# Performance work log

Measured on AMD Instinct MI355X. Metric: run time of the kernel, lower is better.

Reference implementation:

```python
import jax, jax.numpy as jnp
import numpy as np

T, B, C, H, W = 128, 16, 4, 84, 84
NUM_ACTIONS, FEAT, HID = 18, 512, 256


def _conv(x, w, b, stride):
    # x: (N,C,H,W), w: (O,I,kh,kw)
    y = jax.lax.conv_general_dilated(
        x, w, window_strides=(stride, stride), padding='VALID',
        dimension_numbers=('NCHW', 'OIHW', 'NCHW'))
    return y + b[None, :, None, None]


def setup_inputs() -> dict:
    key = jax.random.key(0)
    ks = jax.random.split(key, 24)
    s = 0.05
    inp = {
        'obs_seq': jax.random.uniform(ks[0], (T, B, C, H, W), jnp.float32) * 255.0,
        'actions_seq': jax.random.randint(ks[1], (T, B), 0, NUM_ACTIONS),
        'episode_starts_seq': jax.random.randint(ks[2], (T, B), 0, 2).astype(jnp.float32),
        'h0': jnp.zeros((1, B, HID), jnp.float32),
        'c0': jnp.zeros((1, B, HID), jnp.float32),
        # NatureCNN params
        'conv1_w': jax.random.normal(ks[3], (32, C, 8, 8)) * s,
        'conv1_b': jnp.zeros((32,)),
        'conv2_w': jax.random.normal(ks[4], (64, 32, 4, 4)) * s,
        'conv2_b': jnp.zeros((64,)),
        'conv3_w': jax.random.normal(ks[5], (64, 64, 3, 3)) * s,
        'conv3_b': jnp.zeros((64,)),
        'fc_w': jax.random.normal(ks[6], (FEAT, 64 * 7 * 7)) * s,
        'fc_b': jnp.zeros((FEAT,)),
        # LSTM params (torch gate order i,f,g,o)
        'w_ih': jax.random.normal(ks[7], (4 * HID, FEAT)) * s,
        'w_hh': jax.random.normal(ks[8], (4 * HID, HID)) * s,
        'b_ih': jnp.zeros((4 * HID,)),
        'b_hh': jnp.zeros((4 * HID,)),
        # heads
        'actor_w': jax.random.normal(ks[9], (NUM_ACTIONS, HID)) * 0.01,
        'actor_b': jnp.zeros((NUM_ACTIONS,)),
        'critic_w': jax.random.normal(ks[10], (1, HID)) * s,
        'critic_b': jnp.zeros((1,)),
        'aux_w': jax.random.normal(ks[11], (1, FEAT)) * s,
        'aux_b': jnp.zeros((1,)),
    }
    return inp


def reference(obs_seq, actions_seq, episode_starts_seq, h0, c0,
              conv1_w, conv1_b, conv2_w, conv2_b, conv3_w, conv3_b,
              fc_w, fc_b, w_ih, w_hh, b_ih, b_hh,
              actor_w, actor_b, critic_w, critic_b, aux_w, aux_b):
    t, b = actions_seq.shape
    x = obs_seq.reshape(t * b, *obs_seq.shape[2:]) / 255.0
    x = jax.nn.relu(_conv(x, conv1_w, conv1_b, 4))   # (TB,32,20,20)
    x = jax.nn.relu(_conv(x, conv2_w, conv2_b, 2))   # (TB,64,9,9)
    x = jax.nn.relu(_conv(x, conv3_w, conv3_b, 1))   # (TB,64,7,7)
    feat = jax.nn.relu(x.reshape(t * b, -1) @ fc_w.T + fc_b)  # (TB,FEAT)

    aux_logits = (feat @ aux_w.T + aux_b).squeeze(-1).reshape(t, b)
    feat_seq = feat.reshape(t, b, -1)

    def step(carry, inp):
        h, c = carry
        x_t, s_t = inp
        keep = (1.0 - s_t)[:, None]
        h = h * keep
        c = c * keep
        gates = x_t @ w_ih.T + b_ih + h @ w_hh.T + b_hh  # (B,4H)
        i, f, g, o = jnp.split(gates, 4, axis=-1)
        c = jax.nn.sigmoid(f) * c + jax.nn.sigmoid(i) * jnp.tanh(g)
        h = jax.nn.sigmoid(o) * jnp.tanh(c)
        return (h, c), h

    _, out = jax.lax.scan(step, (h0[0], c0[0]), (feat_seq, episode_starts_seq))  # (T,B,HID)

    logits = out @ actor_w.T + actor_b
    logp = jax.nn.log_softmax(logits, axis=-1)
    log_probs = jnp.take_along_axis(logp, actions_seq[..., None], axis=-1).squeeze(-1)
    entropy = -jnp.sum(jnp.exp(logp) * logp, axis=-1)
    values = (out @ critic_w.T + critic_b).squeeze(-1)
    return log_probs, entropy, values, aux_logits
```

## Files before the change

### kernel.cpp

```cpp
#include <hip/hip_runtime.h>
#include <hip/hip_bf16.h>
#include <cstddef>

typedef __attribute__((ext_vector_type(8))) short bf16x8;
typedef __attribute__((ext_vector_type(4))) float f32x4;

static constexpr size_t OFF_X1B   = 0;
static constexpr size_t OFF_X2B   = 52428800;
static constexpr size_t OFF_X3B   = 73662464;
static constexpr size_t OFF_FEATB = 86507520;
static constexpr size_t OFF_W2B   = 88604672;
static constexpr size_t OFF_W3B   = 88670208;
static constexpr size_t OFF_FCWB  = 88743936;
static constexpr size_t OFF_WIHB  = 91955200;
static constexpr size_t OFF_FEAT  = 93003776;
static constexpr size_t OFF_GX    = 97198080;
static constexpr size_t OFF_HSEQ  = 105586688;
static constexpr size_t OFF_W1B   = 108732416;
static constexpr size_t OFF_WHHB  = 108748800;
static constexpr size_t OFF_ORDB  = 109273088;
static constexpr size_t OFF_ORDT0 = 109281280;
static constexpr size_t OFF_ORDLEN= 109289472;
static constexpr size_t OFF_NSEG  = 109297664;

__device__ __forceinline__ float sigmoidf_(float x) {
  return 1.0f / (1.0f + __expf(-x));
}
__device__ __forceinline__ float tanhf_(float x) {
  return 1.0f - 2.0f / (__expf(2.0f * x) + 1.0f);
}

__global__ __launch_bounds__(256) void prep_kernel(
    const float* __restrict__ c1w, const float* __restrict__ c2w,
    const float* __restrict__ c3w, const float* __restrict__ fcw,
    const float* __restrict__ wih, const float* __restrict__ whh,
    __hip_bfloat16* __restrict__ w1b,
    __hip_bfloat16* __restrict__ w2b, __hip_bfloat16* __restrict__ w3b,
    __hip_bfloat16* __restrict__ fcwb, __hip_bfloat16* __restrict__ wihb,
    __hip_bfloat16* __restrict__ whhb) {
  int i = blockIdx.x * 256 + threadIdx.x;
  if (i < 32768) {
    int o = i >> 9, k = i & 511;
    int pos = k >> 5, ci = k & 31;
    int ky = pos >> 2, kx = pos & 3;
    w2b[i] = __float2bfloat16(c2w[o * 512 + ci * 16 + ky * 4 + kx]);
  } else if (i < 69632) {
    int j = i - 32768;
    int o = j / 576, k = j - o * 576;
    int pos = k >> 6, ci = k & 63;
    int ky = pos / 3, kx = pos - ky * 3;
    w3b[j] = __float2bfloat16(c3w[o * 576 + ci * 9 + ky * 3 + kx]);
  } else if (i < 1675264) {
    int j = i - 69632;
    int o = j / 3136, k = j - o * 3136;
    int sp = k >> 6, ci = k & 63;
    fcwb[j] = __float2bfloat16(fcw[o * 3136 + ci * 49 + sp]);
  } else if (i < 2199552) {
    int j = i - 1675264;
    wihb[j] = __float2bfloat16(wih[j]);
  } else if (i < 2461696) {
    int j = i - 2199552;
    whhb[j] = __float2bfloat16(whh[j]);
  } else if (i < 2469888) {
    int j = i - 2461696;
    int oc = j >> 8, k = j & 255;
    int ky = k >> 5, rem = k & 31;
    int ci = rem >> 3, kx = rem & 7;
    w1b[j] = __float2bfloat16(c1w[oc * 256 + ci * 64 + ky * 8 + kx] * (1.0f / 255.0f));
  }
}

__global__ __launch_bounds__(256) void plan_kernel(
    const float* __restrict__ starts, int* __restrict__ ord_b,
    int* __restrict__ ord_t0, int* __restrict__ ord_len,
    int* __restrict__ nseg_out) {
  __shared__ int s_t0[2048];
  __shared__ int s_len[2048];
  __shared__ int cnt[16];
  __shared__ int hist[132];
  __shared__ int off[132];
  const int tid = threadIdx.x;
  if (tid < 16) {
    int b = tid, c = 0;
    for (int t = 0; t < 128; ++t) {
      float s = starts[t * 16 + b];
      if (t == 0 || s != 0.0f) {
        if (c > 0) s_len[b * 128 + c - 1] = t - s_t0[b * 128 + c - 1];
        s_t0[b * 128 + c] = t;
        ++c;
      }
    }
    s_len[b * 128 + c - 1] = 128 - s_t0[b * 128 + c - 1];
    cnt[b] = c;
  }
  if (tid < 132) hist[tid] = 0;
  __syncthreads();
  for (int idx = tid; idx < 2048; idx += 256) {
    int b = idx >> 7, i = idx & 127;
    if (i < cnt[b]) atomicAdd(&hist[s_len[idx]], 1);
  }
  __syncthreads();
  if (tid == 0) {
    int running = 0;
    for (int L = 128; L >= 1; --L) { off[L] = running; running += hist[L]; }
    *nseg_out = running;
  }
  __syncthreads();
  for (int idx = tid; idx < 2048; idx += 256) {
    int b = idx >> 7, i = idx & 127;
    if (i < cnt[b]) {
      int len = s_len[idx];
      int pos = atomicAdd(&off[len], 1);
      ord_b[pos] = b;
      ord_t0[pos] = s_t0[idx];
      ord_len[pos] = len;
    }
  }
}

__global__ __launch_bounds__(256) void conv1_mfma(
    const float* __restrict__ obs, const __hip_bfloat16* __restrict__ w1b,
    const float* __restrict__ b1, __hip_bfloat16* __restrict__ x1b) {
  constexpr int LDK = 40;
  __shared__ __align__(16) __hip_bfloat16 As[128 * LDK];
  __shared__ __align__(16) __hip_bfloat16 Ws[32 * LDK];
  const int tid = threadIdx.x;
  const int m0 = blockIdx.x * 128;
  const int l = tid & 63;
  const int wv = tid >> 6;
  const int lane16 = l & 15;
  const int quad = l >> 4;
  const int m_base = wv * 32;

  f32x4 acc[2][2] = {};

  const float* arow[2];
  int arw[2], acp[2];
#pragma unroll
  for (int c = 0; c < 2; ++c) {
    const int id = tid + c * 256;
    const int row = id >> 2, cpos = id & 3;
    arw[c] = row; acp[c] = cpos;
    const int m = m0 + row;
    const int n = m / 400, sp = m - n * 400;
    const int oy = sp / 20, ox = sp - oy * 20;
    arow[c] = obs + (size_t)n * 28224 + cpos * 7056 + (oy * 4) * 84 + ox * 4;
  }
  const int wrow = tid >> 2, wcp = tid & 3;
  const __hip_bfloat16* wsrc = w1b + wrow * 256 + wcp * 8;

  for (int s = 0; s < 8; ++s) {
    float4 p[2], q[2];
#pragma unroll
    for (int c = 0; c < 2; ++c) {
      const float* r = arow[c] + s * 84;
      p[c] = *(const float4*)r;
      q[c] = *(const float4*)(r + 4);
    }
    uint4 wval;
    if (tid < 128) wval = *(const uint4*)(wsrc + s * 32);
    __syncthreads();
#pragma unroll
    for (int c = 0; c < 2; ++c) {
      __hip_bfloat16* d = &As[arw[c] * LDK + acp[c] * 8];
      d[0] = __float2bfloat16(p[c].x); d[1] = __float2bfloat16(p[c].y);
      d[2] = __float2bfloat16(p[c].z); d[3] = __float2bfloat16(p[c].w);
      d[4] = __float2bfloat16(q[c].x); d[5] = __float2bfloat16(q[c].y);
      d[6] = __float2bfloat16(q[c].z); d[7] = __float2bfloat16(q[c].w);
    }
    if (tid < 128) *(uint4*)&Ws[wrow * LDK + wcp * 8] = wval;
    __syncthreads();
    const bf16x8 a0 = *(const bf16x8*)&As[(m_base + lane16) * LDK + quad * 8];
    const bf16x8 a1 = *(const bf16x8*)&As[(m_base + 16 + lane16) * LDK + quad * 8];
#pragma unroll
    for (int nf = 0; nf < 2; ++nf) {
      const bf16x8 b = *(const bf16x8*)&Ws[(nf * 16 + lane16) * LDK + quad * 8];
      acc[0][nf] = __builtin_amdgcn_mfma_f32_16x16x32_bf16(a0, b, acc[0][nf], 0, 0, 0);
      acc[1][nf] = __builtin_amdgcn_mfma_f32_16x16x32_bf16(a1, b, acc[1][nf], 0, 0, 0);
    }
  }
#pragma unroll
  for (int nf = 0; nf < 2; ++nf) {
    const int col = nf * 16 + lane16;
    const float bb = b1[col];
#pragma unroll
    for (int mf = 0; mf < 2; ++mf) {
#pragma unroll
      for (int r = 0; r < 4; ++r) {
        const int row = m0 + m_base + mf * 16 + quad * 4 + r;
        const float v = fmaxf(acc[mf][nf][r] + bb, 0.f);
        x1b[(size_t)row * 32 + col] = __float2bfloat16(v);
      }
    }
  }
}

template<int BM, int MODE>
__global__ __launch_bounds__(256) void gemm_mfma(
    const __hip_bfloat16* __restrict__ Abase,
    const __hip_bfloat16* __restrict__ Wb,
    const float* __restrict__ bias1, const float* __restrict__ bias2,
    float* __restrict__ Cf, __hip_bfloat16* __restrict__ Cb,
    const int M, const int N, const int K, const int relu) {
  constexpr int LDK = 40;
  __shared__ __align__(16) __hip_bfloat16 As[BM * LDK];
  __shared__ __align__(16) __hip_bfloat16 Ws[64 * LDK];
  const int tid = threadIdx.x;
  const int m0 = blockIdx.y * BM;
  const int n0 = blockIdx.x * 64;
  const int l = tid & 63;
  const int wv = tid >> 6;
  const int lane16 = l & 15;
  const int quad = l >> 4;
  constexpr int NF = (BM == 128) ? 4 : 2;
  const int m_base = (BM == 128) ? wv * 32 : (wv & 1) * 32;
  const int n_base = (BM == 128) ? 0 : (wv >> 1) * 32;
  constexpr int NCA = (BM == 128) ? 2 : 1;

  f32x4 acc[2][NF] = {};

  const __hip_bfloat16* arow[NCA];
  int acp[NCA];
#pragma unroll
  for (int c = 0; c < NCA; ++c) {
    const int id = tid + c * 256;
    const int row = id >> 2, cpos = id & 3;
    const int m = m0 + row;
    acp[c] = cpos;
    if (MODE == 0) {
      arow[c] = Abase + (size_t)m * K + cpos * 8;
    } else if (MODE == 1) {
      const int n = m / 81, sp = m - n * 81;
      const int oy = sp / 9, ox = sp - oy * 9;
      arow[c] = Abase + ((n * 20 + oy * 2) * 20 + ox * 2) * 32 + cpos * 8;
    } else {
      const int n = m / 49, sp = m - n * 49;
      const int oy = sp / 7, ox = sp - oy * 7;
      arow[c] = Abase + ((n * 9 + oy) * 9 + ox) * 64 + cpos * 8;
    }
  }
  const int wrow = tid >> 2, wcp = tid & 3;
  const __hip_bfloat16* wsrc = Wb + (size_t)(n0 + wrow) * K + wcp * 8;

  const int ksteps = K >> 5;
  for (int s = 0; s < ksteps; ++s) {
    uint4 av[NCA];
#pragma unroll
    for (int c = 0; c < NCA; ++c) {
      const __hip_bfloat16* p;
      if (MODE == 0) {
        p = arow[c] + s * 32;
      } else if (MODE == 1) {
        p = arow[c] + ((s >> 2) * 20 + (s & 3)) * 32;
      } else {
        const int pos = s >> 1;
        const int ky = pos / 3, kx = pos - ky * 3;
        p = arow[c] + (ky * 9 + kx) * 64 + (s & 1) * 32;
      }
      av[c] = *(const uint4*)p;
    }
    const uint4 wval = *(const uint4*)(wsrc + s * 32);
    __syncthreads();
#pragma unroll
    for (int c = 0; c < NCA; ++c) {
      const int row = (tid + c * 256) >> 2;
      *(uint4*)&As[row * LDK + acp[c] * 8] = av[c];
    }
    *(uint4*)&Ws[wrow * LDK + wcp * 8] = wval;
    __syncthreads();
    const bf16x8 a0 = *(const bf16x8*)&As[(m_base + lane16) * LDK + quad * 8];
    const bf16x8 a1 = *(const bf16x8*)&As[(m_base + 16 + lane16) * LDK + quad * 8];
#pragma unroll
    for (int nf = 0; nf < NF; ++nf) {
      const bf16x8 b = *(const bf16x8*)&Ws[(n_base + nf * 16 + lane16) * LDK + quad * 8];
      acc[0][nf] = __builtin_amdgcn_mfma_f32_16x16x32_bf16(a0, b, acc[0][nf], 0, 0, 0);
      acc[1][nf] = __builtin_amdgcn_mfma_f32_16x16x32_bf16(a1, b, acc[1][nf], 0, 0, 0);
    }
  }
#pragma unroll
  for (int nf = 0; nf < NF; ++nf) {
    const int col = n0 + n_base + nf * 16 + lane16;
    float bb = bias1[col];
    if (bias2) bb += bias2[col];
#pragma unroll
    for (int mf = 0; mf < 2; ++mf) {
#pragma unroll
      for (int r = 0; r < 4; ++r) {
        const int row = m0 + m_base + mf * 16 + quad * 4 + r;
        float v = acc[mf][nf][r] + bb;
        if (relu) v = fmaxf(v, 0.f);
        if (Cf) Cf[(size_t)row * N + col] = v;
        if (Cb) Cb[(size_t)row * N + col] = __float2bfloat16(v);
      }
    }
  }
}

__global__ __launch_bounds__(1024, 4) void lstm_mfma(
    const float* __restrict__ gx, const __hip_bfloat16* __restrict__ whhb,
    const float* __restrict__ starts, const float* __restrict__ h0,
    const float* __restrict__ c0, const int* __restrict__ ord_b,
    const int* __restrict__ ord_t0, const int* __restrict__ ord_len,
    const int* __restrict__ nseg_p, float* __restrict__ hseq) {
  constexpr int LDH = 264;
  constexpr int PS  = 1028;
  __shared__ __align__(16) __hip_bfloat16 h_lds[16 * LDH];
  __shared__ __align__(16) float pre[16 * PS];
  __shared__ int sg_b[16], sg_t0[16], sg_len[16];
  const int g = blockIdx.x;
  const int nseg = *nseg_p;
  if (g * 16 >= nseg) return;
  const int tid = threadIdx.x;
  const int wv = tid >> 6;
  const int l = tid & 63;
  const int lane16 = l & 15, quad = l >> 4;
  if (tid < 16) {
    const int s = g * 16 + tid;
    sg_b[tid] = (s < nseg) ? ord_b[s] : 0;
    sg_t0[tid] = (s < nseg) ? ord_t0[s] : 0;
    sg_len[tid] = (s < nseg) ? ord_len[s] : 0;
  }
  __syncthreads();
  bf16x8 bfrag[2][8];
#pragma unroll
  for (int nt = 0; nt < 2; ++nt)
#pragma unroll
    for (int ks = 0; ks < 8; ++ks)
      bfrag[nt][ks] = *(const bf16x8*)&whhb[
          (size_t)(wv * 64 + nt * 16 + lane16) * 256 + ks * 32 + quad * 8];
  const __hip_bfloat16* bs2 = &whhb[(size_t)(wv * 64 + 32 + lane16) * 256 + quad * 8];
  const __hip_bfloat16* bs3 = &whhb[(size_t)(wv * 64 + 48 + lane16) * 256 + quad * 8];

  const int m_own = wv;
  const int u = l * 4;
  const int b_own = sg_b[m_own];
  const int t0_own = sg_t0[m_own];
  const int len_own = sg_len[m_own];
  float4 c_reg = make_float4(0.f, 0.f, 0.f, 0.f);
  {
    float4 hv = make_float4(0.f, 0.f, 0.f, 0.f);
    if (len_own > 0 && t0_own == 0) {
      const float keep = 1.0f - starts[b_own];
      const float4 h4 = *(const float4*)&h0[b_own * 256 + u];
      const float4 c4 = *(const float4*)&c0[b_own * 256 + u];
      hv = make_float4(h4.x * keep, h4.y * keep, h4.z * keep, h4.w * keep);
      c_reg = make_float4(c4.x * keep, c4.y * keep, c4.z * keep, c4.w * keep);
    }
    __hip_bfloat16* hd = &h_lds[m_own * LDH + u];
    hd[0] = __float2bfloat16(hv.x); hd[1] = __float2bfloat16(hv.y);
    hd[2] = __float2bfloat16(hv.z); hd[3] = __float2bfloat16(hv.w);
  }
  const int maxlen = sg_len[0];
  for (int tt = 0; tt < maxlen; ++tt) {
    __syncthreads();
    f32x4 acc[4] = {};
#pragma unroll
    for (int ks = 0; ks < 8; ++ks) {
      const bf16x8 b2 = *(const bf16x8*)(bs2 + ks * 32);
      const bf16x8 b3 = *(const bf16x8*)(bs3 + ks * 32);
      const bf16x8 a = *(const bf16x8*)&h_lds[lane16 * LDH + ks * 32 + quad * 8];
      acc[0] = __builtin_amdgcn_mfma_f32_16x16x32_bf16(a, bfrag[0][ks], acc[0], 0, 0, 0);
      acc[1] = __builtin_amdgcn_mfma_f32_16x16x32_bf16(a, bfrag[1][ks], acc[1], 0, 0, 0);
      acc[2] = __builtin_amdgcn_mfma_f32_16x16x32_bf16(a, b2, acc[2], 0, 0, 0);
      acc[3] = __builtin_amdgcn_mfma_f32_16x16x32_bf16(a, b3, acc[3], 0, 0, 0);
    }
#pragma unroll
    for (int nt = 0; nt < 4; ++nt)
#pragma unroll
      for (int r = 0; r < 4; ++r)
        pre[(quad * 4 + r) * PS + wv * 64 + nt * 16 + lane16] = acc[nt][r];
    __syncthreads();
    if (tt < len_own) {
      const int t = t0_own + tt;
      const size_t gbase = (size_t)(t * 16 + b_own) * 1024 + u;
      const float4 g0 = *(const float4*)&gx[gbase];
      const float4 g1 = *(const float4*)&gx[gbase + 256];
      const float4 g2 = *(const float4*)&gx[gbase + 512];
      const float4 g3 = *(const float4*)&gx[gbase + 768];
      const float4 p0 = *(const float4*)&pre[m_own * PS + u];
      const float4 p1 = *(const float4*)&pre[m_own * PS + u + 256];
      const float4 p2 = *(const float4*)&pre[m_own * PS + u + 512];
      const float4 p3 = *(const float4*)&pre[m_own * PS + u + 768];
      const float i0 = sigmoidf_(p0.x + g0.x), i1 = sigmoidf_(p0.y + g0.y),
                  i2 = sigmoidf_(p0.z + g0.z), i3 = sigmoidf_(p0.w + g0.w);
      const float f0 = sigmoidf_(p1.x + g1.x), f1 = sigmoidf_(p1.y + g1.y),
                  f2 = sigmoidf_(p1.z + g1.z), f3 = sigmoidf_(p1.w + g1.w);
      const float q0 = tanhf_(p2.x + g2.x), q1 = tanhf_(p2.y + g2.y),
                  q2 = tanhf_(p2.z + g2.z), q3 = tanhf_(p2.w + g2.w);
      const float o0 = sigmoidf_(p3.x + g3.x), o1 = sigmoidf_(p3.y + g3.y),
                  o2 = sigmoidf_(p3.z + g3.z), o3 = sigmoidf_(p3.w + g3.w);
      c_reg.x = fmaf(f0, c_reg.x, i0 * q0);
      c_reg.y = fmaf(f1, c_reg.y, i1 * q1);
      c_reg.z = fmaf(f2, c_reg.z, i2 * q2);
      c_reg.w = fmaf(f3, c_reg.w, i3 * q3);
      const float4 h4 = make_float4(o0 * tanhf_(c_reg.x), o1 * tanhf_(c_reg.y),
                                    o2 * tanhf_(c_reg.z), o3 * tanhf_(c_reg.w));
      __hip_bfloat16* hd = &h_lds[m_own * LDH + u];
      hd[0] = __float2bfloat16(h4.x); hd[1] = __float2bfloat16(h4.y);
      hd[2] = __float2bfloat16(h4.z); hd[3] = __float2bfloat16(h4.w);
      *(float4*)&hseq[(size_t)(t * 16 + b_own) * 256 + u] = h4;
    }
  }
}

__global__ __launch_bounds__(256) void aux_kernel(
    const float* __restrict__ feat, const float* __restrict__ aux_w,
    const float* __restrict__ aux_b, float* __restrict__ outp) {
  const int tb = blockIdx.x;
  const int tid = threadIdx.x;
  __shared__ float red[256];
  const float* f = feat + (size_t)tb * 512;
  red[tid] = f[tid] * aux_w[tid] + f[tid + 256] * aux_w[tid + 256];
  __syncthreads();
  for (int s = 128; s > 0; s >>= 1) {
    if (tid < s) red[tid] += red[tid + s];
    __syncthreads();
  }
  if (tid == 0) outp[6144 + tb] = red[0] + aux_b[0];
}

__global__ __launch_bounds__(256) void heads_kernel(
    const float* __restrict__ hseq, const int* __restrict__ actions,
    const float* __restrict__ actor_w, const float* __restrict__ actor_b,
    const float* __restrict__ critic_w, const float* __restrict__ critic_b,
    float* __restrict__ outp) {
  const int tid = threadIdx.x;
  const int wv = tid >> 6, l = tid & 63;
  const int tb = blockIdx.x * 4 + wv;
  const float4 h4 = *(const float4*)&hseq[(size_t)tb * 256 + l * 4];
  float part[19];
#pragma unroll
  for (int o = 0; o < 18; ++o) {
    const float4 w = *(const float4*)&actor_w[o * 256 + l * 4];
    part[o] = h4.x * w.x + h4.y * w.y + h4.z * w.z + h4.w * w.w;
  }
  {
    const float4 w = *(const float4*)&critic_w[l * 4];
    part[18] = h4.x * w.x + h4.y * w.y + h4.z * w.z + h4.w * w.w;
  }
#pragma unroll
  for (int off = 32; off > 0; off >>= 1) {
#pragma unroll
    for (int o = 0; o < 19; ++o) part[o] += __shfl_xor(part[o], off);
  }
  float lg[18];
  float m = -1e30f;
#pragma unroll
  for (int o = 0; o < 18; ++o) {
    lg[o] = part[o] + actor_b[o];
    m = fmaxf(m, lg[o]);
  }
  float se = 0.f;
#pragma unroll
  for (int o = 0; o < 18; ++o) se += __expf(lg[o] - m);
  const float lse = __logf(se);
  float ent = 0.f;
#pragma unroll
  for (int o = 0; o < 18; ++o) {
    const float lp = lg[o] - m - lse;
    ent -= __expf(lp) * lp;
  }
  if (l == 0) {
    const int a = actions[tb];
    outp[tb] = lg[a] - m - lse;
    outp[2048 + tb] = ent;
    outp[4096 + tb] = part[18] + critic_b[0];
  }
}

extern "C" void kernel_launch(void* const* d_in, const int* in_sizes, int n_in,
                              void* d_out, int out_size, void* d_ws, size_t ws_size,
                              hipStream_t stream) {
  const float* obs     = (const float*)d_in[0];
  const int*   actions = (const int*)d_in[1];
  const float* starts  = (const float*)d_in[2];
  const float* h0      = (const float*)d_in[3];
  const float* c0      = (const float*)d_in[4];
  const float* c1w     = (const float*)d_in[5];
  const float* c1b     = (const float*)d_in[6];
  const float* c2w     = (const float*)d_in[7];
  const float* c2b     = (const float*)d_in[8];
  const float* c3w     = (const float*)d_in[9];
  const float* c3b     = (const float*)d_in[10];
  const float* fcw     = (const float*)d_in[11];
  const float* fcb     = (const float*)d_in[12];
  const float* wih     = (const float*)d_in[13];
  const float* whh     = (const float*)d_in[14];
  const float* bih     = (const float*)d_in[15];
  const float* bhh     = (const float*)d_in[16];
  const float* aw      = (const float*)d_in[17];
  const float* ab      = (const float*)d_in[18];
  const float* cw      = (const float*)d_in[19];
  const float* cb      = (const float*)d_in[20];
  const float* auxw    = (const float*)d_in[21];
  const float* auxb    = (const float*)d_in[22];

  char* ws = (char*)d_ws;
  __hip_bfloat16* x1b   = (__hip_bfloat16*)(ws + OFF_X1B);
  __hip_bfloat16* x2b   = (__hip_bfloat16*)(ws + OFF_X2B);
  __hip_bfloat16* x3b   = (__hip_bfloat16*)(ws + OFF_X3B);
  __hip_bfloat16* featb = (__hip_bfloat16*)(ws + OFF_FEATB);
  __hip_bfloat16* w2b   = (__hip_bfloat16*)(ws + OFF_W2B);
  __hip_bfloat16* w3b   = (__hip_bfloat16*)(ws + OFF_W3B);
  __hip_bfloat16* fcwb  = (__hip_bfloat16*)(ws + OFF_FCWB);
  __hip_bfloat16* wihb  = (__hip_bfloat16*)(ws + OFF_WIHB);
  __hip_bfloat16* w1b   = (__hip_bfloat16*)(ws + OFF_W1B);
  __hip_bfloat16* whhb  = (__hip_bfloat16*)(ws + OFF_WHHB);
  float* feat = (float*)(ws + OFF_FEAT);
  float* gx   = (float*)(ws + OFF_GX);
  float* hseq = (float*)(ws + OFF_HSEQ);
  int* ord_b   = (int*)(ws + OFF_ORDB);
  int* ord_t0  = (int*)(ws + OFF_ORDT0);
  int* ord_len = (int*)(ws + OFF_ORDLEN);
  int* nseg    = (int*)(ws + OFF_NSEG);
  float* outp = (float*)d_out;

  prep_kernel<<<9648, 256, 0, stream>>>(c1w, c2w, c3w, fcw, wih, whh,
                                        w1b, w2b, w3b, fcwb, wihb, whhb);
  plan_kernel<<<1, 256, 0, stream>>>(starts, ord_b, ord_t0, ord_len, nseg);
  conv1_mfma<<<6400, 256, 0, stream>>>(obs, w1b, c1b, x1b);
  gemm_mfma<128, 1><<<dim3(1, 1296), 256, 0, stream>>>(
      x1b, w2b, c2b, nullptr, nullptr, x2b, 165888, 64, 512, 1);
  gemm_mfma<128, 2><<<dim3(1, 784), 256, 0, stream>>>(
      x2b, w3b, c3b, nullptr, nullptr, x3b, 100352, 64, 576, 1);
  gemm_mfma<64, 0><<<dim3(8, 32), 256, 0, stream>>>(
      x3b, fcwb, fcb, nullptr, feat, featb, 2048, 512, 3136, 1);
  gemm_mfma<64, 0><<<dim3(16, 32), 256, 0, stream>>>(
      featb, wihb, bih, bhh, gx, nullptr, 2048, 1024, 512, 0);
  aux_kernel<<<2048, 256, 0, stream>>>(feat, auxw, auxb, outp);
  lstm_mfma<<<128, 1024, 0, stream>>>(gx, whhb, starts, h0, c0,
                                      ord_b, ord_t0, ord_len, nseg, hseq);
  heads_kernel<<<512, 256, 0, stream>>>(hseq, actions, aw, ab, cw, cb, outp);
}
```

Measured before the change: 776.3 us.

## Split-K the FC GEMM and fuse its reduction with bias, ReLU and aux head

The FC GEMM (K=3136) originally launched only 256 blocks. It now splits K four ways across blockIdx.z and writes fp32 partial sums. A new fc_reduce kernel adds the four partials, applies bias and ReLU, writes the bf16 features, and computes the aux logit, which removes the separate aux kernel and the fp32 feat buffer. The conv1 A-tile stores are packed into single 16-byte writes, and plan_kernel now stages the episode starts in shared memory first. The cost is extra global traffic for the 4x2048x512 partial buffer and one more kernel launch.

```diff
diff --git a/kernel.cpp b/kernel.cpp
--- a/kernel.cpp
+++ b/kernel.cpp
@@ -3,6 +3,7 @@
 #include <cstddef>
 
 typedef __attribute__((ext_vector_type(8))) short bf16x8;
+typedef __attribute__((ext_vector_type(8))) unsigned short u16x8;
 typedef __attribute__((ext_vector_type(4))) float f32x4;
 
 static constexpr size_t OFF_X1B   = 0;
@@ -13,7 +14,6 @@
 static constexpr size_t OFF_W3B   = 88670208;
 static constexpr size_t OFF_FCWB  = 88743936;
 static constexpr size_t OFF_WIHB  = 91955200;
-static constexpr size_t OFF_FEAT  = 93003776;
 static constexpr size_t OFF_GX    = 97198080;
 static constexpr size_t OFF_HSEQ  = 105586688;
 static constexpr size_t OFF_W1B   = 108732416;
@@ -22,12 +22,18 @@
 static constexpr size_t OFF_ORDT0 = 109281280;
 static constexpr size_t OFF_ORDLEN= 109289472;
 static constexpr size_t OFF_NSEG  = 109297664;
+static constexpr size_t OFF_FCPART= 109305856;
 
 __device__ __forceinline__ float sigmoidf_(float x) {
   return 1.0f / (1.0f + __expf(-x));
 }
 __device__ __forceinline__ float tanhf_(float x) {
   return 1.0f - 2.0f / (__expf(2.0f * x) + 1.0f);
+}
+__device__ __forceinline__ unsigned short f2bfu(float x) {
+  union { __hip_bfloat16 b; unsigned short u; } cv;
+  cv.b = __float2bfloat16(x);
+  return cv.u;
 }
 
 __global__ __launch_bounds__(256) void prep_kernel(
@@ -74,16 +80,25 @@
     const float* __restrict__ starts, int* __restrict__ ord_b,
     int* __restrict__ ord_t0, int* __restrict__ ord_len,
     int* __restrict__ nseg_out) {
+  __shared__ float s_starts[2048];
   __shared__ int s_t0[2048];
   __shared__ int s_len[2048];
   __shared__ int cnt[16];
   __shared__ int hist[132];
   __shared__ int off[132];
   const int tid = threadIdx.x;
+  {
+    float4* d = (float4*)s_starts;
+    const float4* s = (const float4*)starts;
+#pragma unroll
+    for (int i = 0; i < 2; ++i) d[tid + i * 256] = s[tid + i * 256];
+  }
+  if (tid < 132) hist[tid] = 0;
+  __syncthreads();
   if (tid < 16) {
     int b = tid, c = 0;
     for (int t = 0; t < 128; ++t) {
-      float s = starts[t * 16 + b];
+      float s = s_starts[t * 16 + b];
       if (t == 0 || s != 0.0f) {
         if (c > 0) s_len[b * 128 + c - 1] = t - s_t0[b * 128 + c - 1];
         s_t0[b * 128 + c] = t;
@@ -93,7 +108,6 @@
     s_len[b * 128 + c - 1] = 128 - s_t0[b * 128 + c - 1];
     cnt[b] = c;
   }
-  if (tid < 132) hist[tid] = 0;
   __syncthreads();
   for (int idx = tid; idx < 2048; idx += 256) {
     int b = idx >> 7, i = idx & 127;
@@ -162,11 +176,12 @@
     __syncthreads();
 #pragma unroll
     for (int c = 0; c < 2; ++c) {
-      __hip_bfloat16* d = &As[arw[c] * LDK + acp[c] * 8];
-      d[0] = __float2bfloat16(p[c].x); d[1] = __float2bfloat16(p[c].y);
-      d[2] = __float2bfloat16(p[c].z); d[3] = __float2bfloat16(p[c].w);
-      d[4] = __float2bfloat16(q[c].x); d[5] = __float2bfloat16(q[c].y);
-      d[6] = __float2bfloat16(q[c].z); d[7] = __float2bfloat16(q[c].w);
+      u16x8 v;
+      v[0] = f2bfu(p[c].x); v[1] = f2bfu(p[c].y);
+      v[2] = f2bfu(p[c].z); v[3] = f2bfu(p[c].w);
+      v[4] = f2bfu(q[c].x); v[5] = f2bfu(q[c].y);
+      v[6] = f2bfu(q[c].z); v[7] = f2bfu(q[c].w);
+      *(u16x8*)&As[arw[c] * LDK + acp[c] * 8] = v;
     }
     if (tid < 128) *(uint4*)&Ws[wrow * LDK + wcp * 8] = wval;
     __syncthreads();
@@ -201,7 +216,8 @@
     const __hip_bfloat16* __restrict__ Wb,
     const float* __restrict__ bias1, const float* __restrict__ bias2,
     float* __restrict__ Cf, __hip_bfloat16* __restrict__ Cb,
-    const int M, const int N, const int K, const int relu) {
+    const int M, const int N, const int K, const int relu,
+    float* __restrict__ Cpart) {
   constexpr int LDK = 40;
   __shared__ __align__(16) __hip_bfloat16 As[BM * LDK];
   __shared__ __align__(16) __hip_bfloat16 Ws[64 * LDK];
@@ -242,8 +258,15 @@
   const int wrow = tid >> 2, wcp = tid & 3;
   const __hip_bfloat16* wsrc = Wb + (size_t)(n0 + wrow) * K + wcp * 8;
 
-  const int ksteps = K >> 5;
-  for (int s = 0; s < ksteps; ++s) {
+  int s0 = 0, s1 = K >> 5;
+  if (Cpart) {
+    const int total = K >> 5;
+    const int zz = blockIdx.z;
+    const int q = total >> 2, rr = total & 3;
+    s0 = zz * q + (zz < rr ? zz : rr);
+    s1 = s0 + q + (zz < rr ? 1 : 0);
+  }
+  for (int s = s0; s < s1; ++s) {
     uint4 av[NCA];
 #pragma unroll
     for (int c = 0; c < NCA; ++c) {
@@ -277,6 +300,22 @@
       acc[1][nf] = __builtin_amdgcn_mfma_f32_16x16x32_bf16(a1, b, acc[1][nf], 0, 0, 0);
     }
   }
+  if (Cpart) {
+    float* dst = Cpart + (size_t)blockIdx.z * M * N;
+#pragma unroll
+    for (int nf = 0; nf < NF; ++nf) {
+      const int col = n0 + n_base + nf * 16 + lane16;
+#pragma unroll
+      for (int mf = 0; mf < 2; ++mf) {
+#pragma unroll
+        for (int r = 0; r < 4; ++r) {
+          const int row = m0 + m_base + mf * 16 + quad * 4 + r;
+          dst[(size_t)row * N + col] = acc[mf][nf][r];
+        }
+      }
+    }
+    return;
+  }
 #pragma unroll
   for (int nf = 0; nf < NF; ++nf) {
     const int col = n0 + n_base + nf * 16 + lane16;
@@ -294,6 +333,34 @@
       }
     }
   }
+}
+
+__global__ __launch_bounds__(256) void fc_reduce(
+    const float* __restrict__ part, const float* __restrict__ fcb,
+    const float* __restrict__ aux_w, const float* __restrict__ aux_b,
+    __hip_bfloat16* __restrict__ featb, float* __restrict__ outp) {
+  const int row = blockIdx.x;
+  const int tid = threadIdx.x;
+  __shared__ float red[256];
+  float auxacc = 0.f;
+#pragma unroll
+  for (int h = 0; h < 2; ++h) {
+    const int c = tid + h * 256;
+    const size_t base = (size_t)row * 512 + c;
+    float v = part[base] + part[1048576 + base] + part[2097152 + base] +
+              part[3145728 + base];
+    v += fcb[c];
+    v = fmaxf(v, 0.f);
+    featb[base] = __float2bfloat16(v);
+    auxacc += v * aux_w[c];
+  }
+  red[tid] = auxacc;
+  __syncthreads();
+  for (int s = 128; s > 0; s >>= 1) {
+    if (tid < s) red[tid] += red[tid + s];
+    __syncthreads();
+  }
+  if (tid == 0) outp[6144 + row] = red[0] + aux_b[0];
 }
 
 __global__ __launch_bounds__(1024, 4) void lstm_mfma(
@@ -403,22 +470,6 @@
   }
 }
 
-__global__ __launch_bounds__(256) void aux_kernel(
-    const float* __restrict__ feat, const float* __restrict__ aux_w,
-    const float* __restrict__ aux_b, float* __restrict__ outp) {
-  const int tb = blockIdx.x;
-  const int tid = threadIdx.x;
-  __shared__ float red[256];
-  const float* f = feat + (size_t)tb * 512;
-  red[tid] = f[tid] * aux_w[tid] + f[tid + 256] * aux_w[tid + 256];
-  __syncthreads();
-  for (int s = 128; s > 0; s >>= 1) {
-    if (tid < s) red[tid] += red[tid + s];
-    __syncthreads();
-  }
-  if (tid == 0) outp[6144 + tb] = red[0] + aux_b[0];
-}
-
 __global__ __launch_bounds__(256) void heads_kernel(
     const float* __restrict__ hseq, const int* __restrict__ actions,
     const float* __restrict__ actor_w, const float* __restrict__ actor_b,
@@ -506,13 +557,13 @@
   __hip_bfloat16* wihb  = (__hip_bfloat16*)(ws + OFF_WIHB);
   __hip_bfloat16* w1b   = (__hip_bfloat16*)(ws + OFF_W1B);
   __hip_bfloat16* whhb  = (__hip_bfloat16*)(ws + OFF_WHHB);
-  float* feat = (float*)(ws + OFF_FEAT);
   float* gx   = (float*)(ws + OFF_GX);
   float* hseq = (float*)(ws + OFF_HSEQ);
   int* ord_b   = (int*)(ws + OFF_ORDB);
   int* ord_t0  = (int*)(ws + OFF_ORDT0);
   int* ord_len = (int*)(ws + OFF_ORDLEN);
   int* nseg    = (int*)(ws + OFF_NSEG);
+  float* fcpart= (float*)(ws + OFF_FCPART);
   float* outp = (float*)d_out;
 
   prep_kernel<<<9648, 256, 0, stream>>>(c1w, c2w, c3w, fcw, wih, whh,
@@ -520,14 +571,14 @@
   plan_kernel<<<1, 256, 0, stream>>>(starts, ord_b, ord_t0, ord_len, nseg);
   conv1_mfma<<<6400, 256, 0, stream>>>(obs, w1b, c1b, x1b);
   gemm_mfma<128, 1><<<dim3(1, 1296), 256, 0, stream>>>(
-      x1b, w2b, c2b, nullptr, nullptr, x2b, 165888, 64, 512, 1);
+      x1b, w2b, c2b, nullptr, nullptr, x2b, 165888, 64, 512, 1, nullptr);
   gemm_mfma<128, 2><<<dim3(1, 784), 256, 0, stream>>>(
-      x2b, w3b, c3b, nullptr, nullptr, x3b, 100352, 64, 576, 1);
-  gemm_mfma<64, 0><<<dim3(8, 32), 256, 0, stream>>>(
-      x3b, fcwb, fcb, nullptr, feat, featb, 2048, 512, 3136, 1);
+      x2b, w3b, c3b, nullptr, nullptr, x3b, 100352, 64, 576, 1, nullptr);
+  gemm_mfma<64, 0><<<dim3(8, 32, 4), 256, 0, stream>>>(
+      x3b, fcwb, fcb, nullptr, nullptr, nullptr, 2048, 512, 3136, 0, fcpart);
+  fc_reduce<<<2048, 256, 0, stream>>>(fcpart, fcb, auxw, auxb, featb, outp);
   gemm_mfma<64, 0><<<dim3(16, 32), 256, 0, stream>>>(
-      featb, wihb, bih, bhh, gx, nullptr, 2048, 1024, 512, 0);
-  aux_kernel<<<2048, 256, 0, stream>>>(feat, auxw, auxb, outp);
+      featb, wihb, bih, bhh, gx, nullptr, 2048, 1024, 512, 0, nullptr);
   lstm_mfma<<<128, 1024, 0, stream>>>(gx, whhb, starts, h0, c0,
                                       ord_b, ord_t0, ord_len, nseg, hseq);
   heads_kernel<<<512, 256, 0, stream>>>(hseq, actions, aw, ab, cw, cb, outp);
```

New measurement: 722.5 us. 1.07x faster.
